# Performance work log

Hardware: AMD Instinct MI355X
Metric: run time of the kernel (lower is better)

Reference implementation:

```python
import jax, jax.numpy as jnp
import numpy as np

N, E, EL = 20000, 320000, 100000
IN, HID, OUT, H = 256, 128, 128, 4
NEG_SLOPE = 0.2


def setup_inputs() -> dict:
    key = jax.random.key(0)
    ks = jax.random.split(key, 20)
    g = lambda k, shape, fan: jax.random.normal(k, shape, jnp.float32) * (1.0 / np.sqrt(fan))
    inp = {
        'x': jax.random.normal(ks[0], (N, IN), jnp.float32),
        'edge_index': jax.random.randint(ks[1], (2, E), 0, N, jnp.int32),
        'edge_label_index': jax.random.randint(ks[2], (2, EL), 0, N, jnp.int32),
        # GATv2 layer 1: in -> hidden, heads=H, concat
        'W_l1': g(ks[3], (IN, H * HID), IN), 'b_l1': jnp.zeros((H * HID,), jnp.float32),
        'W_r1': g(ks[4], (IN, H * HID), IN), 'b_r1': jnp.zeros((H * HID,), jnp.float32),
        'att1': g(ks[5], (H, HID), HID), 'bias1': jnp.zeros((H * HID,), jnp.float32),
        # GATv2 layer 2: H*hidden -> out, heads=1
        'W_l2': g(ks[6], (H * HID, OUT), H * HID), 'b_l2': jnp.zeros((OUT,), jnp.float32),
        'W_r2': g(ks[7], (H * HID, OUT), H * HID), 'b_r2': jnp.zeros((OUT,), jnp.float32),
        'att2': g(ks[8], (1, OUT), OUT), 'bias2': jnp.zeros((OUT,), jnp.float32),
        # decoder: Linear(2*OUT, HID) -> GELU -> Linear(HID, 1)
        'W_d1': g(ks[9], (2 * OUT, HID), 2 * OUT), 'b_d1': jnp.zeros((HID,), jnp.float32),
        'W_d2': g(ks[10], (HID, 1), HID), 'b_d2': jnp.zeros((1,), jnp.float32),
    }
    return inp


def gatv2_conv(x, src, dst, Wl, bl, Wr, br, att, bias, heads, ch):
    n = x.shape[0]
    xl = (x @ Wl + bl).reshape(n, heads, ch)  # source transform
    xr = (x @ Wr + br).reshape(n, heads, ch)  # target transform
    xj = xl[src]                              # [E, H, C] messages from source
    xi = xr[dst]                              # [E, H, C]
    e = jax.nn.leaky_relu(xi + xj, NEG_SLOPE)
    logits = jnp.einsum('ehc,hc->eh', e, att)  # [E, H]
    # segment softmax over incoming edges of each target node
    m = jax.ops.segment_max(logits, dst, num_segments=n)
    a = jnp.exp(logits - m[dst])
    s = jax.ops.segment_sum(a, dst, num_segments=n)
    alpha = a / s[dst]
    out = jax.ops.segment_sum(alpha[..., None] * xj, dst, num_segments=n)
    return out.reshape(n, heads * ch) + bias


def reference(x, edge_index, edge_label_index,
              W_l1, b_l1, W_r1, b_r1, att1, bias1,
              W_l2, b_l2, W_r2, b_r2, att2, bias2,
              W_d1, b_d1, W_d2, b_d2):
    n = x.shape[0]
    loops = jnp.arange(n, dtype=edge_index.dtype)
    src = jnp.concatenate([edge_index[0], loops])  # add_self_loops=True (PyG default)
    dst = jnp.concatenate([edge_index[1], loops])
    z = gatv2_conv(x, src, dst, W_l1, b_l1, W_r1, b_r1, att1, bias1, H, HID)
    z = jax.nn.gelu(z)  # dropout is identity in eval mode
    z = gatv2_conv(z, src, dst, W_l2, b_l2, W_r2, b_r2, att2, bias2, 1, OUT)
    # link decoder: gather-concat-MLP
    h = jnp.concatenate([z[edge_label_index[0]], z[edge_label_index[1]]], axis=-1)
    h = jax.nn.gelu(h @ W_d1 + b_d1)
    return (h @ W_d2 + b_d2).squeeze(-1)
```

## Files before the change

### kernel.cpp

```cpp
#include <hip/hip_runtime.h>
#include <hip/hip_bf16.h>
#include <math.h>
#include <stdint.h>

using bf16 = __hip_bfloat16;
typedef unsigned short u16;
typedef unsigned int   u32;
typedef __attribute__((ext_vector_type(8))) short short8;
typedef __attribute__((ext_vector_type(4))) float f32x4;

static constexpr int NN   = 20000;
static constexpr int EE   = 320000;
static constexpr int ELN  = 100000;
static constexpr int ETOT = EE + NN;
static constexpr int INC  = 256;
static constexpr int C1   = 512;
static constexpr int C2   = 128;
static constexpr int NB   = (NN + 255) / 256;

__device__ __forceinline__ float us2f(u16 u){ union{u32 i; float f;}x; x.i=((u32)u)<<16; return x.f; }
__device__ __forceinline__ u16  f2us(float f){ union{bf16 h; u16 u;}c; c.h=__float2bfloat16(f); return c.u; }
__device__ __forceinline__ float h2f(u16 u){ union{u16 u; _Float16 h;}c; c.u=u; return (float)c.h; }
__device__ __forceinline__ float gelu_f(float x){
  float u = 1.5957691216057308f*(x + 0.044715f*x*x*x);
  float ex = __expf(u);
  float th = 1.f - 2.f/(ex + 1.f);
  return 0.5f*x*(1.f+th);
}
__device__ __forceinline__ void ld4v(const float* p, float* o){ float4 v=*(const float4*)p; o[0]=v.x;o[1]=v.y;o[2]=v.z;o[3]=v.w; }
__device__ __forceinline__ void ld4v(const u16* p, float* o){ uint2 v=*(const uint2*)p;
  o[0]=us2f(v.x&0xffff);o[1]=us2f(v.x>>16);o[2]=us2f(v.y&0xffff);o[3]=us2f(v.y>>16); }
__device__ __forceinline__ void ld4v(const _Float16* p, float* o){ uint2 v=*(const uint2*)p;
  o[0]=h2f(v.x&0xffff);o[1]=h2f(v.x>>16);o[2]=h2f(v.y&0xffff);o[3]=h2f(v.y>>16); }
__device__ __forceinline__ void ld8v(const float* p, float* o){ ld4v(p,o); ld4v(p+4,o+4); }
__device__ __forceinline__ void ld8v(const u16* p, float* o){ uint4 v=*(const uint4*)p;
  o[0]=us2f(v.x&0xffff);o[1]=us2f(v.x>>16);o[2]=us2f(v.y&0xffff);o[3]=us2f(v.y>>16);
  o[4]=us2f(v.z&0xffff);o[5]=us2f(v.z>>16);o[6]=us2f(v.w&0xffff);o[7]=us2f(v.w>>16); }
__device__ __forceinline__ void ld8v(const _Float16* p, float* o){ uint4 v=*(const uint4*)p;
  o[0]=h2f(v.x&0xffff);o[1]=h2f(v.x>>16);o[2]=h2f(v.y&0xffff);o[3]=h2f(v.y>>16);
  o[4]=h2f(v.z&0xffff);o[5]=h2f(v.z>>16);o[6]=h2f(v.w&0xffff);o[7]=h2f(v.w>>16); }
__device__ __forceinline__ void ld2v(const float* p, float* o){ float2 v=*(const float2*)p; o[0]=v.x;o[1]=v.y; }
__device__ __forceinline__ void ld2v(const _Float16* p, float* o){ u32 w=*(const u32*)p;
  o[0]=h2f(w&0xffff); o[1]=h2f(w>>16); }
__device__ __forceinline__ void st4v(float* p, const float* v){ *(float4*)p = make_float4(v[0],v[1],v[2],v[3]); }
__device__ __forceinline__ void st4v(u16* p, const float* v){ uint2 o;
  o.x=f2us(v[0])|((u32)f2us(v[1])<<16); o.y=f2us(v[2])|((u32)f2us(v[3])<<16); *(uint2*)p=o; }
__device__ __forceinline__ void st8v(float* p, const float* v){ st4v(p,v); st4v(p+4,v+4); }
__device__ __forceinline__ void st8v(u16* p, const float* v){ uint4 o;
  o.x=f2us(v[0])|((u32)f2us(v[1])<<16); o.y=f2us(v[2])|((u32)f2us(v[3])<<16);
  o.z=f2us(v[4])|((u32)f2us(v[5])<<16); o.w=f2us(v[6])|((u32)f2us(v[7])<<16); *(uint4*)p=o; }
__device__ __forceinline__ void st8v(_Float16* p, const float* v){
  union{ _Float16 h[8]; uint4 u; } c;
  #pragma unroll
  for (int j=0;j<8;++j) c.h[j] = (_Float16)v[j];
  *(uint4*)p = c.u; }

__global__ void k_hist(const int* __restrict__ ei, int* __restrict__ cnt) {
  int e = blockIdx.x*blockDim.x + threadIdx.x;
  if (e < ETOT) {
    int d = (e < EE) ? ei[EE + e] : (e - EE);
    if ((u32)d < (u32)NN) atomicAdd(&cnt[d], 1);
  }
}
__global__ void k_scan_a(const int* __restrict__ cnt, int* __restrict__ row_ptr,
                         int* __restrict__ bsum) {
  __shared__ int buf[256];
  int idx = blockIdx.x*256 + threadIdx.x;
  int v = (idx < NN) ? cnt[idx] : 0;
  buf[threadIdx.x] = v;
  __syncthreads();
  for (int off = 1; off < 256; off <<= 1) {
    int t = (threadIdx.x >= off) ? buf[threadIdx.x - off] : 0;
    __syncthreads();
    buf[threadIdx.x] += t;
    __syncthreads();
  }
  if (idx < NN) row_ptr[idx] = buf[threadIdx.x] - v;
  if (threadIdx.x == 255) bsum[blockIdx.x] = buf[255];
}
__global__ void k_scan_b(int* __restrict__ bsum, int* __restrict__ row_ptr) {
  __shared__ int buf[128];
  int v = (threadIdx.x < NB) ? bsum[threadIdx.x] : 0;
  buf[threadIdx.x] = v;
  __syncthreads();
  for (int off = 1; off < 128; off <<= 1) {
    int t = (threadIdx.x >= off) ? buf[threadIdx.x - off] : 0;
    __syncthreads();
    buf[threadIdx.x] += t;
    __syncthreads();
  }
  if (threadIdx.x < NB) bsum[threadIdx.x] = buf[threadIdx.x] - v;
  if (threadIdx.x == 127) row_ptr[NN] = buf[127];
}
__global__ void k_scan_c(int* __restrict__ row_ptr, const int* __restrict__ bsum,
                         int* __restrict__ cur) {
  int idx = blockIdx.x*256 + threadIdx.x;
  if (idx < NN) {
    int v = row_ptr[idx] + bsum[blockIdx.x];
    row_ptr[idx] = v;
    cur[idx] = v;
  }
}
__global__ void k_scatter(const int* __restrict__ ei, int* __restrict__ cur,
                          int* __restrict__ col) {
  int e = blockIdx.x*blockDim.x + threadIdx.x;
  if (e < ETOT) {
    int s, d;
    if (e < EE) { s = ei[e]; d = ei[EE + e]; } else { s = d = e - EE; }
    if ((u32)d >= (u32)NN) d = 0;
    int pos = atomicAdd(&cur[d], 1);
    if ((u32)pos < (u32)ETOT) col[pos] = s;
  }
}

struct WsArgs { const float* src[5]; u16* th[5]; u16* tl[5]; int K[5]; int N[5]; };
__global__ __launch_bounds__(256) void k_wsplit_all(WsArgs a) {
  int seg = blockIdx.y;
  int K = a.K[seg], N = a.N[seg];
  int n = K * N;
  int idx = blockIdx.x*256 + threadIdx.x;
  if (idx >= n) return;
  int nn = idx / K, k = idx - nn*K;
  float v = a.src[seg][(size_t)k*N + nn];
  u16 h = f2us(v);
  a.th[seg][idx] = h;
  a.tl[seg][idx] = f2us(v - us2f(h));
}

template <typename AT, typename CT>
__global__ __launch_bounds__(256, 2)
void k_mgemm(const AT* __restrict__ A,
             const u16* __restrict__ Bth, const u16* __restrict__ Btl,
             const float* __restrict__ bias, CT* __restrict__ C,
             int M, int N, int K) {
  __shared__ __align__(16) u16 Ah[128][32], Al[128][32];
  __shared__ __align__(16) u16 Bh[128][32], Bl[128][32];
  int tid = threadIdx.x;
  int m0 = blockIdx.x * 128, n0 = blockIdx.y * 128;
  int wave = tid >> 6, lane = tid & 63;
  int wm = (wave & 1) * 64, wn = (wave >> 1) * 64;
  int l15 = lane & 15, quad = lane >> 4;
  f32x4 acc[4][4] = {};
  int ar = tid >> 3;
  int ak = (tid & 7) * 4;
  int bn = tid >> 2;
  int bc = (tid & 3) * 8;
  for (int k0 = 0; k0 < K; k0 += 32) {
    #pragma unroll
    for (int i = 0; i < 4; ++i) {
      int row = ar + 32*i;
      int gr = m0 + row;
      float hv[4] = {0.f, 0.f, 0.f, 0.f};
      if (gr < M) ld4v(&A[(size_t)gr*K + k0 + ak], hv);
      u16 hi[4], lo[4];
      #pragma unroll
      for (int j = 0; j < 4; ++j) {
        hi[j] = f2us(hv[j]);
        lo[j] = f2us(hv[j] - us2f(hi[j]));
      }
      *(uint2*)&Ah[row][ak] = make_uint2(hi[0]|((u32)hi[1]<<16), hi[2]|((u32)hi[3]<<16));
      *(uint2*)&Al[row][ak] = make_uint2(lo[0]|((u32)lo[1]<<16), lo[2]|((u32)lo[3]<<16));
    }
    #pragma unroll
    for (int i = 0; i < 2; ++i) {
      int n = bn + 64*i;
      *(uint4*)&Bh[n][bc] = *(const uint4*)&Bth[(size_t)(n0+n)*K + k0 + bc];
      *(uint4*)&Bl[n][bc] = *(const uint4*)&Btl[(size_t)(n0+n)*K + k0 + bc];
    }
    __syncthreads();
    short8 af_h[4], af_l[4], bf_h[4], bf_l[4];
    #pragma unroll
    for (int i = 0; i < 4; ++i) {
      af_h[i] = *(const short8*)&Ah[wm + i*16 + l15][quad*8];
      af_l[i] = *(const short8*)&Al[wm + i*16 + l15][quad*8];
      bf_h[i] = *(const short8*)&Bh[wn + i*16 + l15][quad*8];
      bf_l[i] = *(const short8*)&Bl[wn + i*16 + l15][quad*8];
    }
    #pragma unroll
    for (int i = 0; i < 4; ++i)
      #pragma unroll
      for (int j = 0; j < 4; ++j) {
        acc[i][j] = __builtin_amdgcn_mfma_f32_16x16x32_bf16(af_h[i], bf_l[j], acc[i][j], 0,0,0);
        acc[i][j] = __builtin_amdgcn_mfma_f32_16x16x32_bf16(af_l[i], bf_h[j], acc[i][j], 0,0,0);
        acc[i][j] = __builtin_amdgcn_mfma_f32_16x16x32_bf16(af_h[i], bf_h[j], acc[i][j], 0,0,0);
      }
    __syncthreads();
  }
  #pragma unroll
  for (int j = 0; j < 4; ++j) {
    int col = n0 + wn + j*16 + l15;
    float bv = bias[col];
    #pragma unroll
    for (int i = 0; i < 4; ++i) {
      int rbase = m0 + wm + i*16 + quad*4;
      #pragma unroll
      for (int r = 0; r < 4; ++r) {
        int row = rbase + r;
        if (row < M) C[(size_t)row*N + col] = (CT)(acc[i][j][r] + bv);
      }
    }
  }
}

__global__ __launch_bounds__(256, 2)
void k_dec3(const _Float16* __restrict__ z2,
            const int* __restrict__ eli,
            const u16* __restrict__ Wth, const u16* __restrict__ Wtl,
            const float* __restrict__ bd1,
            const float* __restrict__ Wd2, const float* __restrict__ bd2,
            float* __restrict__ out) {
  __shared__ __align__(16) u16 Ah[128][32], Al[128][32];
  __shared__ __align__(16) u16 Bh[128][32], Bl[128][32];
  __shared__ float pr[128][2];
  int tid = threadIdx.x;
  int e0 = blockIdx.x * 128;
  int wave = tid >> 6, lane = tid & 63;
  int wm = (wave & 1) * 64, wn = (wave >> 1) * 64;
  int l15 = lane & 15, quad = lane >> 4;
  int ar = tid >> 3;
  int ak = (tid & 7) * 4;
  int bn = tid >> 2;
  int bc = (tid & 3) * 8;
  int ia4[4], ib4[4];
  #pragma unroll
  for (int i = 0; i < 4; ++i) {
    int e = e0 + ar + 32*i;
    bool ev = e < ELN;
    int a = ev ? eli[e] : 0;      if ((u32)a >= (u32)NN) a = 0;
    int b = ev ? eli[ELN+e] : 0;  if ((u32)b >= (u32)NN) b = 0;
    ia4[i] = a; ib4[i] = b;
  }
  f32x4 acc[4][4] = {};
  for (int k0 = 0; k0 < 256; k0 += 32) {
    #pragma unroll
    for (int i = 0; i < 4; ++i) {
      int row = ar + 32*i;
      int kk = k0 + ak;
      const _Float16* src = (kk < 128) ? &z2[(size_t)ia4[i]*128 + kk]
                                       : &z2[(size_t)ib4[i]*128 + (kk - 128)];
      float hv[4];
      ld4v(src, hv);
      u16 hi[4], lo[4];
      #pragma unroll
      for (int j = 0; j < 4; ++j) {
        hi[j] = f2us(hv[j]);
        lo[j] = f2us(hv[j] - us2f(hi[j]));
      }
      *(uint2*)&Ah[row][ak] = make_uint2(hi[0]|((u32)hi[1]<<16), hi[2]|((u32)hi[3]<<16));
      *(uint2*)&Al[row][ak] = make_uint2(lo[0]|((u32)lo[1]<<16), lo[2]|((u32)lo[3]<<16));
    }
    #pragma unroll
    for (int i = 0; i < 2; ++i) {
      int n = bn + 64*i;
      *(uint4*)&Bh[n][bc] = *(const uint4*)&Wth[(size_t)n*256 + k0 + bc];
      *(uint4*)&Bl[n][bc] = *(const uint4*)&Wtl[(size_t)n*256 + k0 + bc];
    }
    __syncthreads();
    short8 af_h[4], af_l[4], bf_h[4], bf_l[4];
    #pragma unroll
    for (int i = 0; i < 4; ++i) {
      af_h[i] = *(const short8*)&Ah[wm + i*16 + l15][quad*8];
      af_l[i] = *(const short8*)&Al[wm + i*16 + l15][quad*8];
      bf_h[i] = *(const short8*)&Bh[wn + i*16 + l15][quad*8];
      bf_l[i] = *(const short8*)&Bl[wn + i*16 + l15][quad*8];
    }
    #pragma unroll
    for (int i = 0; i < 4; ++i)
      #pragma unroll
      for (int j = 0; j < 4; ++j) {
        acc[i][j] = __builtin_amdgcn_mfma_f32_16x16x32_bf16(af_h[i], bf_l[j], acc[i][j], 0,0,0);
        acc[i][j] = __builtin_amdgcn_mfma_f32_16x16x32_bf16(af_l[i], bf_h[j], acc[i][j], 0,0,0);
        acc[i][j] = __builtin_amdgcn_mfma_f32_16x16x32_bf16(af_h[i], bf_h[j], acc[i][j], 0,0,0);
      }
    __syncthreads();
  }
  float w2c[4], bbc[4];
  #pragma unroll
  for (int j = 0; j < 4; ++j) {
    int col = wn + j*16 + l15;
    w2c[j] = Wd2[col];
    bbc[j] = bd1[col];
  }
  #pragma unroll
  for (int i = 0; i < 4; ++i) {
    #pragma unroll
    for (int r = 0; r < 4; ++r) {
      float part = 0.f;
      #pragma unroll
      for (int j = 0; j < 4; ++j)
        part += gelu_f(acc[i][j][r] + bbc[j]) * w2c[j];
      part += __shfl_xor(part,1); part += __shfl_xor(part,2);
      part += __shfl_xor(part,4); part += __shfl_xor(part,8);
      if (l15 == 0) pr[wm + i*16 + quad*4 + r][wn>>6] = part;
    }
  }
  __syncthreads();
  if (tid < 128) {
    int e = e0 + tid;
    if (e < ELN) out[e] = pr[tid][0] + pr[tid][1] + bd2[0];
  }
}

template <typename AT, typename CT>
__global__ __launch_bounds__(256) void k_gemm(const AT* __restrict__ A,
                                              const float* __restrict__ W,
                                              const float* __restrict__ bias,
                                              CT* __restrict__ C,
                                              int M, int Nc, int K) {
  __shared__ __align__(16) float As[16][64];
  __shared__ __align__(16) float Bs[16][64];
  int tid = threadIdx.x;
  int m0 = blockIdx.x*64, n0 = blockIdx.y*64;
  int ty = tid >> 4, tx = tid & 15;
  int lrow = tid >> 2;
  int lk   = (tid & 3)*4;
  int wk   = tid >> 4;
  int wn   = (tid & 15)*4;
  float acc[4][4] = {};
  for (int k0 = 0; k0 < K; k0 += 16) {
    int row = m0 + lrow;
    if (row < M) {
      float a4[4]; ld4v(&A[(size_t)row*K + k0 + lk], a4);
      As[lk+0][lrow]=a4[0]; As[lk+1][lrow]=a4[1]; As[lk+2][lrow]=a4[2]; As[lk+3][lrow]=a4[3];
    } else {
      #pragma unroll
      for (int j=0;j<4;++j) As[lk+j][lrow]=0.f;
    }
    {
      float4 bv4 = *(const float4*)&W[(size_t)(k0+wk)*Nc + n0 + wn];
      Bs[wk][wn+0]=bv4.x; Bs[wk][wn+1]=bv4.y; Bs[wk][wn+2]=bv4.z; Bs[wk][wn+3]=bv4.w;
    }
    __syncthreads();
    #pragma unroll
    for (int kk=0;kk<16;++kk) {
      float4 av = *(const float4*)&As[kk][ty*4];
      float4 bv = *(const float4*)&Bs[kk][tx*4];
      float a[4]={av.x,av.y,av.z,av.w}, b[4]={bv.x,bv.y,bv.z,bv.w};
      #pragma unroll
      for (int i=0;i<4;++i)
        #pragma unroll
        for (int j=0;j<4;++j)
          acc[i][j] += a[i]*b[j];
    }
    __syncthreads();
  }
  float bv[4];
  #pragma unroll
  for (int j=0;j<4;++j) bv[j] = bias[n0 + tx*4 + j];
  #pragma unroll
  for (int i=0;i<4;++i) {
    int row = m0 + ty*4 + i;
    if (row < M) {
      float o4[4] = {acc[i][0]+bv[0], acc[i][1]+bv[1], acc[i][2]+bv[2], acc[i][3]+bv[3]};
      st4v(&C[(size_t)row*Nc + n0 + tx*4], o4);
    }
  }
}

template <typename TI, typename TO>
__global__ __launch_bounds__(256) void k_edge1(const TI* __restrict__ xl,
                                               const TI* __restrict__ xr,
                                               const float* __restrict__ att,
                                               const float* __restrict__ bias,
                                               const int* __restrict__ row_ptr,
                                               const int* __restrict__ col,
                                               TO* __restrict__ z1) {
  int wid = (blockIdx.x*blockDim.x + threadIdx.x) >> 6;
  if (wid >= NN) return;
  int lane = threadIdx.x & 63;
  int c8 = lane*8;
  float xi[8], av[8], acc[8] = {};
  ld8v(&xr[(size_t)wid*C1 + c8], xi);
  #pragma unroll
  for (int j=0;j<8;++j) av[j] = att[c8+j];
  float m = -1e30f, s = 0.f;
  int e0 = row_ptr[wid], e1 = row_ptr[wid+1];
  int e = e0;
  if ((e1 - e0) & 1) {
    int sn = col[e]; if ((u32)sn >= (u32)NN) sn = 0;
    float xj[8];
    ld8v(&xl[(size_t)sn*C1 + c8], xj);
    float p = 0.f;
    #pragma unroll
    for (int j=0;j<8;++j) {
      float t = xi[j] + xj[j];
      t = fmaxf(t, 0.2f*t);
      p += t*av[j];
    }
    p += __shfl_xor(p,1); p += __shfl_xor(p,2);
    p += __shfl_xor(p,4); p += __shfl_xor(p,8);
    float mn = fmaxf(m, p);
    float f = __expf(m - mn), w = __expf(p - mn);
    s = s*f + w;
    #pragma unroll
    for (int j=0;j<8;++j) acc[j] = acc[j]*f + w*xj[j];
    m = mn;
    ++e;
  }
  for (; e < e1; e += 2) {
    int s1 = col[e];   if ((u32)s1 >= (u32)NN) s1 = 0;
    int s2 = col[e+1]; if ((u32)s2 >= (u32)NN) s2 = 0;
    float xj1[8], xj2[8];
    ld8v(&xl[(size_t)s1*C1 + c8], xj1);
    ld8v(&xl[(size_t)s2*C1 + c8], xj2);
    float p1 = 0.f, p2 = 0.f;
    #pragma unroll
    for (int j=0;j<8;++j) {
      float t1 = xi[j] + xj1[j]; t1 = fmaxf(t1, 0.2f*t1); p1 += t1*av[j];
      float t2 = xi[j] + xj2[j]; t2 = fmaxf(t2, 0.2f*t2); p2 += t2*av[j];
    }
    p1 += __shfl_xor(p1,1); p2 += __shfl_xor(p2,1);
    p1 += __shfl_xor(p1,2); p2 += __shfl_xor(p2,2);
    p1 += __shfl_xor(p1,4); p2 += __shfl_xor(p2,4);
    p1 += __shfl_xor(p1,8); p2 += __shfl_xor(p2,8);
    float mn = fmaxf(m, fmaxf(p1, p2));
    float f  = __expf(m - mn);
    float w1 = __expf(p1 - mn);
    float w2 = __expf(p2 - mn);
    s = s*f + w1 + w2;
    #pragma unroll
    for (int j=0;j<8;++j) acc[j] = acc[j]*f + (w1*xj1[j] + w2*xj2[j]);
    m = mn;
  }
  float inv = 1.f/s, o[8];
  #pragma unroll
  for (int j=0;j<8;++j) o[j] = gelu_f(acc[j]*inv + bias[c8+j]);
  st8v(&z1[(size_t)wid*C1 + c8], o);
}

template <typename TI, typename TO>
__global__ __launch_bounds__(256) void k_edge2(const TI* __restrict__ xl,
                                               const TI* __restrict__ xr,
                                               const float* __restrict__ att,
                                               const float* __restrict__ bias,
                                               const int* __restrict__ row_ptr,
                                               const int* __restrict__ col,
                                               TO* __restrict__ z2) {
  int wid = (blockIdx.x*blockDim.x + threadIdx.x) >> 6;
  if (wid >= NN) return;
  int lane = threadIdx.x & 63;
  int c2 = lane*2;
  float xiv[2];
  ld2v(&xr[(size_t)wid*C2 + c2], xiv);
  float a0 = att[c2], a1 = att[c2+1];
  float m = -1e30f, s = 0.f, ac0 = 0.f, ac1 = 0.f;
  int e0 = row_ptr[wid], e1 = row_ptr[wid+1];
  int e = e0;
  if ((e1 - e0) & 1) {
    int sn = col[e]; if ((u32)sn >= (u32)NN) sn = 0;
    float xj[2];
    ld2v(&xl[(size_t)sn*C2 + c2], xj);
    float t0 = xiv[0] + xj[0]; t0 = fmaxf(t0, 0.2f*t0);
    float t1 = xiv[1] + xj[1]; t1 = fmaxf(t1, 0.2f*t1);
    float p = t0*a0 + t1*a1;
    p += __shfl_xor(p,1);  p += __shfl_xor(p,2);
    p += __shfl_xor(p,4);  p += __shfl_xor(p,8);
    p += __shfl_xor(p,16); p += __shfl_xor(p,32);
    float mn = fmaxf(m, p);
    float f = __expf(m - mn), w = __expf(p - mn);
    s = s*f + w;
    ac0 = ac0*f + w*xj[0];
    ac1 = ac1*f + w*xj[1];
    m = mn;
    ++e;
  }
  for (; e < e1; e += 2) {
    int s1 = col[e];   if ((u32)s1 >= (u32)NN) s1 = 0;
    int s2 = col[e+1]; if ((u32)s2 >= (u32)NN) s2 = 0;
    float xj1[2], xj2[2];
    ld2v(&xl[(size_t)s1*C2 + c2], xj1);
    ld2v(&xl[(size_t)s2*C2 + c2], xj2);
    float u0 = xiv[0] + xj1[0]; u0 = fmaxf(u0, 0.2f*u0);
    float u1 = xiv[1] + xj1[1]; u1 = fmaxf(u1, 0.2f*u1);
    float v0 = xiv[0] + xj2[0]; v0 = fmaxf(v0, 0.2f*v0);
    float v1 = xiv[1] + xj2[1]; v1 = fmaxf(v1, 0.2f*v1);
    float p1 = u0*a0 + u1*a1;
    float p2 = v0*a0 + v1*a1;
    p1 += __shfl_xor(p1,1);  p2 += __shfl_xor(p2,1);
    p1 += __shfl_xor(p1,2);  p2 += __shfl_xor(p2,2);
    p1 += __shfl_xor(p1,4);  p2 += __shfl_xor(p2,4);
    p1 += __shfl_xor(p1,8);  p2 += __shfl_xor(p2,8);
    p1 += __shfl_xor(p1,16); p2 += __shfl_xor(p2,16);
    p1 += __shfl_xor(p1,32); p2 += __shfl_xor(p2,32);
    float mn = fmaxf(m, fmaxf(p1, p2));
    float f  = __expf(m - mn);
    float w1 = __expf(p1 - mn);
    float w2 = __expf(p2 - mn);
    s = s*f + w1 + w2;
    ac0 = ac0*f + (w1*xj1[0] + w2*xj2[0]);
    ac1 = ac1*f + (w1*xj1[1] + w2*xj2[1]);
    m = mn;
  }
  float inv = 1.f/s;
  z2[(size_t)wid*C2 + c2]   = (TO)(ac0*inv + bias[c2]);
  z2[(size_t)wid*C2 + c2+1] = (TO)(ac1*inv + bias[c2+1]);
}

__global__ __launch_bounds__(256) void k_dec2(const float* __restrict__ z2,
                                              const int* __restrict__ eli,
                                              const float* __restrict__ Wd1,
                                              const float* __restrict__ bd1,
                                              const float* __restrict__ Wd2,
                                              const float* __restrict__ bd2,
                                              float* __restrict__ out) {
  __shared__ __align__(16) float As[16][64];
  __shared__ __align__(16) float Bs[16][128];
  int tid = threadIdx.x;
  int e0 = blockIdx.x * 64;
  int ty = tid >> 4, tx = tid & 15;
  int lrow = tid >> 2;
  int lk   = (tid & 3) * 4;
  int wk   = tid >> 4;
  int wn   = (tid & 15) * 8;
  int e = e0 + lrow;
  bool ev = e < ELN;
  int ia = ev ? eli[e] : 0;       if ((u32)ia >= (u32)NN) ia = 0;
  int ib = ev ? eli[ELN+e] : 0;   if ((u32)ib >= (u32)NN) ib = 0;
  float acc[4][8] = {};
  for (int k0 = 0; k0 < 256; k0 += 16) {
    int kk4 = k0 + lk;
    const float* src = (kk4 < 128) ? &z2[(size_t)ia*128 + kk4]
                                   : &z2[(size_t)ib*128 + (kk4 - 128)];
    float4 a4 = ev ? *(const float4*)src : make_float4(0.f,0.f,0.f,0.f);
    As[lk+0][lrow]=a4.x; As[lk+1][lrow]=a4.y; As[lk+2][lrow]=a4.z; As[lk+3][lrow]=a4.w;
    *(float4*)&Bs[wk][wn]   = *(const float4*)&Wd1[(size_t)(k0+wk)*128 + wn];
    *(float4*)&Bs[wk][wn+4] = *(const float4*)&Wd1[(size_t)(k0+wk)*128 + wn + 4];
    __syncthreads();
    #pragma unroll
    for (int kk = 0; kk < 16; ++kk) {
      float4 av = *(const float4*)&As[kk][ty*4];
      float a[4] = {av.x, av.y, av.z, av.w};
      float4 b0 = *(const float4*)&Bs[kk][tx*4];
      float4 b1 = *(const float4*)&Bs[kk][64 + tx*4];
      float b[8] = {b0.x,b0.y,b0.z,b0.w,b1.x,b1.y,b1.z,b1.w};
      #pragma unroll
      for (int i = 0; i < 4; ++i)
        #pragma unroll
        for (int j = 0; j < 8; ++j)
          acc[i][j] += a[i]*b[j];
    }
    __syncthreads();
  }
  float w2[8], bb[8];
  #pragma unroll
  for (int j = 0; j < 4; ++j) {
    w2[j]   = Wd2[tx*4+j];      bb[j]   = bd1[tx*4+j];
    w2[j+4] = Wd2[64+tx*4+j];   bb[j+4] = bd1[64+tx*4+j];
  }
  float b2 = bd2[0];
  #pragma unroll
  for (int i = 0; i < 4; ++i) {
    float part = 0.f;
    #pragma unroll
    for (int j = 0; j < 8; ++j)
      part += gelu_f(acc[i][j] + bb[j]) * w2[j];
    part += __shfl_xor(part,1); part += __shfl_xor(part,2);
    part += __shfl_xor(part,4); part += __shfl_xor(part,8);
    int row = e0 + ty*4 + i;
    if (tx == 0 && row < ELN) out[row] = part + b2;
  }
}

__global__ void k_tiny(float* out, float code) {
  if (threadIdx.x == 0) out[0] = code;
}

extern "C" void kernel_launch(void* const* d_in, const int* in_sizes, int n_in,
                              void* d_out, int out_size, void* d_ws, size_t ws_size,
                              hipStream_t stream) {
  const float* x     = (const float*)d_in[0];
  const int*   ei    = (const int*)  d_in[1];
  const int*   eli   = (const int*)  d_in[2];
  const float* Wl1   = (const float*)d_in[3];
  const float* bl1   = (const float*)d_in[4];
  const float* Wr1   = (const float*)d_in[5];
  const float* br1   = (const float*)d_in[6];
  const float* att1  = (const float*)d_in[7];
  const float* bias1 = (const float*)d_in[8];
  const float* Wl2   = (const float*)d_in[9];
  const float* bl2   = (const float*)d_in[10];
  const float* Wr2   = (const float*)d_in[11];
  const float* br2   = (const float*)d_in[12];
  const float* att2  = (const float*)d_in[13];
  const float* bias2 = (const float*)d_in[14];
  const float* Wd1   = (const float*)d_in[15];
  const float* bd1   = (const float*)d_in[16];
  const float* Wd2   = (const float*)d_in[17];
  const float* bd2   = (const float*)d_in[18];
  float* out = (float*)d_out;

  constexpr size_t INTW = (size_t)(NN+1) + NN + ETOT;
  constexpr size_t FULL_WORDS = 3ull*NN*C1 + INTW;
  constexpr size_t CMP_WORDS  = 3ull*NN*C1/2 + INTW;

  bool full    = ws_size >= FULL_WORDS*4;
  bool compact = !full && ws_size >= CMP_WORDS*4;
  if (!full && !compact) {
    size_t mb = ws_size >> 20;
    k_tiny<<<1, 64, 0, stream>>>(out, 16384.f + (float)mb);
    return;
  }

  size_t regA = full ? (size_t)NN*C1 : (size_t)NN*C1/2;
  char* base = (char*)d_ws;
  void* wA = base;
  void* wB = base + regA*4;
  void* wC = base + 2*regA*4;
  int* row_ptr = (int*)(base + 3*regA*4);
  int* cnt     = row_ptr + (NN + 1);
  int* col     = cnt + NN;
  int* bsum    = (int*)wA;

  hipMemsetAsync(cnt, 0, NN*sizeof(int), stream);
  k_hist<<<(ETOT+255)/256, 256, 0, stream>>>(ei, cnt);
  k_scan_a<<<NB, 256, 0, stream>>>(cnt, row_ptr, bsum);
  k_scan_b<<<1, 128, 0, stream>>>(bsum, row_ptr);
  k_scan_c<<<NB, 256, 0, stream>>>(row_ptr, bsum, cnt);
  k_scatter<<<(ETOT+255)/256, 256, 0, stream>>>(ei, cnt, col);

  if (full) {
    _Float16* xl1 = (_Float16*)wA;
    _Float16* xr1 = (_Float16*)wB;
    _Float16* z1  = (_Float16*)wC;
    _Float16* xl2 = (_Float16*)wA;
    _Float16* xr2 = (_Float16*)wB;
    _Float16* z2  = (_Float16*)wC;
    u16* wl1th = (u16*)((char*)wB + (21u<<20));
    u16* wl1tl = wl1th + 512*256;
    u16* wr1th = wl1tl + 512*256;
    u16* wr1tl = wr1th + 512*256;
    u16* wl2th = wr1tl + 512*256;
    u16* wl2tl = wl2th + 128*512;
    u16* wr2th = wl2tl + 128*512;
    u16* wr2tl = wr2th + 128*512;
    u16* wdth  = wr2tl + 128*512;
    u16* wdtl  = wdth  + 128*256;

    WsArgs wa;
    wa.src[0]=Wl1; wa.th[0]=wl1th; wa.tl[0]=wl1tl; wa.K[0]=INC; wa.N[0]=C1;
    wa.src[1]=Wr1; wa.th[1]=wr1th; wa.tl[1]=wr1tl; wa.K[1]=INC; wa.N[1]=C1;
    wa.src[2]=Wl2; wa.th[2]=wl2th; wa.tl[2]=wl2tl; wa.K[2]=C1;  wa.N[2]=C2;
    wa.src[3]=Wr2; wa.th[3]=wr2th; wa.tl[3]=wr2tl; wa.K[3]=C1;  wa.N[3]=C2;
    wa.src[4]=Wd1; wa.th[4]=wdth;  wa.tl[4]=wdtl;  wa.K[4]=256; wa.N[4]=C2;
    k_wsplit_all<<<dim3(512, 5), 256, 0, stream>>>(wa);

    dim3 gm1((NN+127)/128, C1/128);
    k_mgemm<float,_Float16><<<gm1, 256, 0, stream>>>(x, wl1th, wl1tl, bl1, xl1, NN, C1, INC);
    k_mgemm<float,_Float16><<<gm1, 256, 0, stream>>>(x, wr1th, wr1tl, br1, xr1, NN, C1, INC);
    k_edge1<_Float16,_Float16><<<NN/4, 256, 0, stream>>>(xl1, xr1, att1, bias1, row_ptr, col, z1);
    dim3 gm2((NN+127)/128, C2/128);
    k_mgemm<_Float16,_Float16><<<gm2, 256, 0, stream>>>(z1, wl2th, wl2tl, bl2, xl2, NN, C2, C1);
    k_mgemm<_Float16,_Float16><<<gm2, 256, 0, stream>>>(z1, wr2th, wr2tl, br2, xr2, NN, C2, C1);
    k_edge2<_Float16,_Float16><<<NN/4, 256, 0, stream>>>(xl2, xr2, att2, bias2, row_ptr, col, z2);
    k_dec3<<<(ELN+127)/128, 256, 0, stream>>>(z2, eli, wdth, wdtl, bd1, Wd2, bd2, out);
  } else {
    u16* xl1 = (u16*)wA;
    u16* xr1 = (u16*)wB;
    u16* z1  = (u16*)wC;
    float* xl2 = (float*)wA;
    float* xr2 = (float*)wB;
    float* z2  = (float*)wC;
    dim3 g1((NN+63)/64, C1/64);
    dim3 g2((NN+63)/64, C2/64);
    k_gemm<float,u16><<<g1, 256, 0, stream>>>(x, Wl1, bl1, xl1, NN, C1, INC);
    k_gemm<float,u16><<<g1, 256, 0, stream>>>(x, Wr1, br1, xr1, NN, C1, INC);
    k_edge1<u16,u16><<<NN/4, 256, 0, stream>>>(xl1, xr1, att1, bias1, row_ptr, col, z1);
    k_gemm<u16,float><<<g2, 256, 0, stream>>>(z1, Wl2, bl2, xl2, NN, C2, C1);
    k_gemm<u16,float><<<g2, 256, 0, stream>>>(z1, Wr2, br2, xr2, NN, C2, C1);
    k_edge2<float,float><<<NN/4, 256, 0, stream>>>(xl2, xr2, att2, bias2, row_ptr, col, z2);
    k_dec2<<<(ELN+63)/64, 256, 0, stream>>>(z2, eli, Wd1, bd1, Wd2, bd2, out);
  }
}
```

Before: 424.4 us.

## Fuse left/right GATv2 projections into one GEMM and drop online-softmax max tracking

Concatenates W_l and W_r into one weight matrix per layer so each layer runs a single wider GEMM producing interleaved xl|xr rows, with the edge kernels reading them through a leading-dimension stride. The first layer's input x is pre-split into bf16 hi/lo once by a new kernel, and a packed-A GEMM variant then loads those halves directly instead of converting fp32 per tile. The edge kernels also drop the running-max rescaling in the segment softmax and exponentiate logits directly, which removes exps and multiplies per edge but can overflow if logits grow large.

```diff
diff --git a/kernel.cpp b/kernel.cpp
--- a/kernel.cpp
+++ b/kernel.cpp
@@ -113,6 +113,17 @@
   }
 }
 
+__global__ __launch_bounds__(256) void k_xsplit(const float* __restrict__ A,
+                                                u16* __restrict__ Ath, u16* __restrict__ Atl,
+                                                int n) {
+  for (int i = blockIdx.x*256 + threadIdx.x; i < n; i += gridDim.x*256) {
+    float v = A[i];
+    u16 h = f2us(v);
+    Ath[i] = h;
+    Atl[i] = f2us(v - us2f(h));
+  }
+}
+
 struct WsArgs { const float* src[5]; u16* th[5]; u16* tl[5]; int K[5]; int N[5]; };
 __global__ __launch_bounds__(256) void k_wsplit_all(WsArgs a) {
   int seg = blockIdx.y;
@@ -127,12 +138,85 @@
   a.tl[seg][idx] = f2us(v - us2f(h));
 }
 
+template <typename CT>
+__global__ __launch_bounds__(256, 2)
+void k_mgemm_p(const u16* __restrict__ Ath, const u16* __restrict__ Atl,
+               const u16* __restrict__ Bth, const u16* __restrict__ Btl,
+               const float* __restrict__ biasA, const float* __restrict__ biasB, int ncut,
+               CT* __restrict__ C, int M, int N, int K) {
+  __shared__ __align__(16) u16 Ah[128][32], Al[128][32];
+  __shared__ __align__(16) u16 Bh[128][32], Bl[128][32];
+  int tid = threadIdx.x;
+  int m0 = blockIdx.x * 128, n0 = blockIdx.y * 128;
+  int wave = tid >> 6, lane = tid & 63;
+  int wm = (wave & 1) * 64, wn = (wave >> 1) * 64;
+  int l15 = lane & 15, quad = lane >> 4;
+  f32x4 acc[4][4] = {};
+  int ar = tid >> 1;
+  int ac = (tid & 1) * 16;
+  int bn = tid >> 2;
+  int bc = (tid & 3) * 8;
+  uint4 z4 = make_uint4(0,0,0,0);
+  for (int k0 = 0; k0 < K; k0 += 32) {
+    int gr = m0 + ar;
+    if (gr < M) {
+      const u16* ph = &Ath[(size_t)gr*K + k0 + ac];
+      const u16* pl = &Atl[(size_t)gr*K + k0 + ac];
+      *(uint4*)&Ah[ar][ac]   = *(const uint4*)ph;
+      *(uint4*)&Ah[ar][ac+8] = *(const uint4*)(ph+8);
+      *(uint4*)&Al[ar][ac]   = *(const uint4*)pl;
+      *(uint4*)&Al[ar][ac+8] = *(const uint4*)(pl+8);
+    } else {
+      *(uint4*)&Ah[ar][ac] = z4; *(uint4*)&Ah[ar][ac+8] = z4;
+      *(uint4*)&Al[ar][ac] = z4; *(uint4*)&Al[ar][ac+8] = z4;
+    }
+    #pragma unroll
+    for (int i = 0; i < 2; ++i) {
+      int n = bn + 64*i;
+      *(uint4*)&Bh[n][bc] = *(const uint4*)&Bth[(size_t)(n0+n)*K + k0 + bc];
+      *(uint4*)&Bl[n][bc] = *(const uint4*)&Btl[(size_t)(n0+n)*K + k0 + bc];
+    }
+    __syncthreads();
+    short8 af_h[4], af_l[4], bf_h[4], bf_l[4];
+    #pragma unroll
+    for (int i = 0; i < 4; ++i) {
+      af_h[i] = *(const short8*)&Ah[wm + i*16 + l15][quad*8];
+      af_l[i] = *(const short8*)&Al[wm + i*16 + l15][quad*8];
+      bf_h[i] = *(const short8*)&Bh[wn + i*16 + l15][quad*8];
+      bf_l[i] = *(const short8*)&Bl[wn + i*16 + l15][quad*8];
+    }
+    #pragma unroll
+    for (int i = 0; i < 4; ++i)
+      #pragma unroll
+      for (int j = 0; j < 4; ++j) {
+        acc[i][j] = __builtin_amdgcn_mfma_f32_16x16x32_bf16(af_h[i], bf_l[j], acc[i][j], 0,0,0);
+        acc[i][j] = __builtin_amdgcn_mfma_f32_16x16x32_bf16(af_l[i], bf_h[j], acc[i][j], 0,0,0);
+        acc[i][j] = __builtin_amdgcn_mfma_f32_16x16x32_bf16(af_h[i], bf_h[j], acc[i][j], 0,0,0);
+      }
+    __syncthreads();
+  }
+  #pragma unroll
+  for (int j = 0; j < 4; ++j) {
+    int col = n0 + wn + j*16 + l15;
+    float bv = (col < ncut) ? biasA[col] : biasB[col - ncut];
+    #pragma unroll
+    for (int i = 0; i < 4; ++i) {
+      int rbase = m0 + wm + i*16 + quad*4;
+      #pragma unroll
+      for (int r = 0; r < 4; ++r) {
+        int row = rbase + r;
+        if (row < M) C[(size_t)row*N + col] = (CT)(acc[i][j][r] + bv);
+      }
+    }
+  }
+}
+
 template <typename AT, typename CT>
 __global__ __launch_bounds__(256, 2)
 void k_mgemm(const AT* __restrict__ A,
              const u16* __restrict__ Bth, const u16* __restrict__ Btl,
-             const float* __restrict__ bias, CT* __restrict__ C,
-             int M, int N, int K) {
+             const float* __restrict__ biasA, const float* __restrict__ biasB, int ncut,
+             CT* __restrict__ C, int M, int N, int K) {
   __shared__ __align__(16) u16 Ah[128][32], Al[128][32];
   __shared__ __align__(16) u16 Bh[128][32], Bl[128][32];
   int tid = threadIdx.x;
@@ -189,7 +273,7 @@
   #pragma unroll
   for (int j = 0; j < 4; ++j) {
     int col = n0 + wn + j*16 + l15;
-    float bv = bias[col];
+    float bv = (col < ncut) ? biasA[col] : biasB[col - ncut];
     #pragma unroll
     for (int i = 0; i < 4; ++i) {
       int rbase = m0 + wm + i*16 + quad*4;
@@ -359,7 +443,7 @@
 
 template <typename TI, typename TO>
 __global__ __launch_bounds__(256) void k_edge1(const TI* __restrict__ xl,
-                                               const TI* __restrict__ xr,
+                                               const TI* __restrict__ xr, int ld,
                                                const float* __restrict__ att,
                                                const float* __restrict__ bias,
                                                const int* __restrict__ row_ptr,
@@ -370,16 +454,16 @@
   int lane = threadIdx.x & 63;
   int c8 = lane*8;
   float xi[8], av[8], acc[8] = {};
-  ld8v(&xr[(size_t)wid*C1 + c8], xi);
+  ld8v(&xr[(size_t)wid*ld + c8], xi);
   #pragma unroll
   for (int j=0;j<8;++j) av[j] = att[c8+j];
-  float m = -1e30f, s = 0.f;
+  float s = 0.f;
   int e0 = row_ptr[wid], e1 = row_ptr[wid+1];
   int e = e0;
   if ((e1 - e0) & 1) {
     int sn = col[e]; if ((u32)sn >= (u32)NN) sn = 0;
     float xj[8];
-    ld8v(&xl[(size_t)sn*C1 + c8], xj);
+    ld8v(&xl[(size_t)sn*ld + c8], xj);
     float p = 0.f;
     #pragma unroll
     for (int j=0;j<8;++j) {
@@ -389,20 +473,18 @@
     }
     p += __shfl_xor(p,1); p += __shfl_xor(p,2);
     p += __shfl_xor(p,4); p += __shfl_xor(p,8);
-    float mn = fmaxf(m, p);
-    float f = __expf(m - mn), w = __expf(p - mn);
-    s = s*f + w;
-    #pragma unroll
-    for (int j=0;j<8;++j) acc[j] = acc[j]*f + w*xj[j];
-    m = mn;
+    float w = __expf(p);
+    s += w;
+    #pragma unroll
+    for (int j=0;j<8;++j) acc[j] += w*xj[j];
     ++e;
   }
   for (; e < e1; e += 2) {
     int s1 = col[e];   if ((u32)s1 >= (u32)NN) s1 = 0;
     int s2 = col[e+1]; if ((u32)s2 >= (u32)NN) s2 = 0;
     float xj1[8], xj2[8];
-    ld8v(&xl[(size_t)s1*C1 + c8], xj1);
-    ld8v(&xl[(size_t)s2*C1 + c8], xj2);
+    ld8v(&xl[(size_t)s1*ld + c8], xj1);
+    ld8v(&xl[(size_t)s2*ld + c8], xj2);
     float p1 = 0.f, p2 = 0.f;
     #pragma unroll
     for (int j=0;j<8;++j) {
@@ -413,14 +495,11 @@
     p1 += __shfl_xor(p1,2); p2 += __shfl_xor(p2,2);
     p1 += __shfl_xor(p1,4); p2 += __shfl_xor(p2,4);
     p1 += __shfl_xor(p1,8); p2 += __shfl_xor(p2,8);
-    float mn = fmaxf(m, fmaxf(p1, p2));
-    float f  = __expf(m - mn);
-    float w1 = __expf(p1 - mn);
-    float w2 = __expf(p2 - mn);
-    s = s*f + w1 + w2;
-    #pragma unroll
-    for (int j=0;j<8;++j) acc[j] = acc[j]*f + (w1*xj1[j] + w2*xj2[j]);
-    m = mn;
+    float w1 = __expf(p1);
+    float w2 = __expf(p2);
+    s += w1 + w2;
+    #pragma unroll
+    for (int j=0;j<8;++j) acc[j] += w1*xj1[j] + w2*xj2[j];
   }
   float inv = 1.f/s, o[8];
   #pragma unroll
@@ -430,7 +509,7 @@
 
 template <typename TI, typename TO>
 __global__ __launch_bounds__(256) void k_edge2(const TI* __restrict__ xl,
-                                               const TI* __restrict__ xr,
+                                               const TI* __restrict__ xr, int ld,
                                                const float* __restrict__ att,
                                                const float* __restrict__ bias,
                                                const int* __restrict__ row_ptr,
@@ -441,35 +520,33 @@
   int lane = threadIdx.x & 63;
   int c2 = lane*2;
   float xiv[2];
-  ld2v(&xr[(size_t)wid*C2 + c2], xiv);
+  ld2v(&xr[(size_t)wid*ld + c2], xiv);
   float a0 = att[c2], a1 = att[c2+1];
-  float m = -1e30f, s = 0.f, ac0 = 0.f, ac1 = 0.f;
+  float s = 0.f, ac0 = 0.f, ac1 = 0.f;
   int e0 = row_ptr[wid], e1 = row_ptr[wid+1];
   int e = e0;
   if ((e1 - e0) & 1) {
     int sn = col[e]; if ((u32)sn >= (u32)NN) sn = 0;
     float xj[2];
-    ld2v(&xl[(size_t)sn*C2 + c2], xj);
+    ld2v(&xl[(size_t)sn*ld + c2], xj);
     float t0 = xiv[0] + xj[0]; t0 = fmaxf(t0, 0.2f*t0);
     float t1 = xiv[1] + xj[1]; t1 = fmaxf(t1, 0.2f*t1);
     float p = t0*a0 + t1*a1;
     p += __shfl_xor(p,1);  p += __shfl_xor(p,2);
     p += __shfl_xor(p,4);  p += __shfl_xor(p,8);
     p += __shfl_xor(p,16); p += __shfl_xor(p,32);
-    float mn = fmaxf(m, p);
-    float f = __expf(m - mn), w = __expf(p - mn);
-    s = s*f + w;
-    ac0 = ac0*f + w*xj[0];
-    ac1 = ac1*f + w*xj[1];
-    m = mn;
+    float w = __expf(p);
+    s += w;
+    ac0 += w*xj[0];
+    ac1 += w*xj[1];
     ++e;
   }
   for (; e < e1; e += 2) {
     int s1 = col[e];   if ((u32)s1 >= (u32)NN) s1 = 0;
     int s2 = col[e+1]; if ((u32)s2 >= (u32)NN) s2 = 0;
     float xj1[2], xj2[2];
-    ld2v(&xl[(size_t)s1*C2 + c2], xj1);
-    ld2v(&xl[(size_t)s2*C2 + c2], xj2);
+    ld2v(&xl[(size_t)s1*ld + c2], xj1);
+    ld2v(&xl[(size_t)s2*ld + c2], xj2);
     float u0 = xiv[0] + xj1[0]; u0 = fmaxf(u0, 0.2f*u0);
     float u1 = xiv[1] + xj1[1]; u1 = fmaxf(u1, 0.2f*u1);
     float v0 = xiv[0] + xj2[0]; v0 = fmaxf(v0, 0.2f*v0);
@@ -482,14 +559,11 @@
     p1 += __shfl_xor(p1,8);  p2 += __shfl_xor(p2,8);
     p1 += __shfl_xor(p1,16); p2 += __shfl_xor(p2,16);
     p1 += __shfl_xor(p1,32); p2 += __shfl_xor(p2,32);
-    float mn = fmaxf(m, fmaxf(p1, p2));
-    float f  = __expf(m - mn);
-    float w1 = __expf(p1 - mn);
-    float w2 = __expf(p2 - mn);
-    s = s*f + w1 + w2;
-    ac0 = ac0*f + (w1*xj1[0] + w2*xj2[0]);
-    ac1 = ac1*f + (w1*xj1[1] + w2*xj2[1]);
-    m = mn;
+    float w1 = __expf(p1);
+    float w2 = __expf(p2);
+    s += w1 + w2;
+    ac0 += w1*xj1[0] + w2*xj2[0];
+    ac1 += w1*xj1[1] + w2*xj2[1];
   }
   float inv = 1.f/s;
   z2[(size_t)wid*C2 + c2]   = (TO)(ac0*inv + bias[c2]);
@@ -619,39 +693,38 @@
   k_scatter<<<(ETOT+255)/256, 256, 0, stream>>>(ei, cnt, col);
 
   if (full) {
-    _Float16* xl1 = (_Float16*)wA;
-    _Float16* xr1 = (_Float16*)wB;
-    _Float16* z1  = (_Float16*)wC;
-    _Float16* xl2 = (_Float16*)wA;
-    _Float16* xr2 = (_Float16*)wB;
-    _Float16* z2  = (_Float16*)wC;
-    u16* wl1th = (u16*)((char*)wB + (21u<<20));
-    u16* wl1tl = wl1th + 512*256;
-    u16* wr1th = wl1tl + 512*256;
-    u16* wr1tl = wr1th + 512*256;
-    u16* wl2th = wr1tl + 512*256;
-    u16* wl2tl = wl2th + 128*512;
-    u16* wr2th = wl2tl + 128*512;
-    u16* wr2tl = wr2th + 128*512;
-    u16* wdth  = wr2tl + 128*512;
+    _Float16* xlr1 = (_Float16*)wA;
+    _Float16* z1   = (_Float16*)wC;
+    _Float16* xlr2 = (_Float16*)wA;
+    _Float16* z2   = (_Float16*)wC;
+    u16* xth = (u16*)wB;
+    u16* xtl = xth + (size_t)NN*INC;
+    u16* wt1th = (u16*)((char*)wB + (21u<<20));
+    u16* wt1tl = wt1th + 1024*256;
+    u16* wt2th = wt1tl + 1024*256;
+    u16* wt2tl = wt2th + 256*512;
+    u16* wdth  = wt2tl + 256*512;
     u16* wdtl  = wdth  + 128*256;
 
+    k_xsplit<<<2048, 256, 0, stream>>>(x, xth, xtl, NN*INC);
     WsArgs wa;
-    wa.src[0]=Wl1; wa.th[0]=wl1th; wa.tl[0]=wl1tl; wa.K[0]=INC; wa.N[0]=C1;
-    wa.src[1]=Wr1; wa.th[1]=wr1th; wa.tl[1]=wr1tl; wa.K[1]=INC; wa.N[1]=C1;
-    wa.src[2]=Wl2; wa.th[2]=wl2th; wa.tl[2]=wl2tl; wa.K[2]=C1;  wa.N[2]=C2;
-    wa.src[3]=Wr2; wa.th[3]=wr2th; wa.tl[3]=wr2tl; wa.K[3]=C1;  wa.N[3]=C2;
-    wa.src[4]=Wd1; wa.th[4]=wdth;  wa.tl[4]=wdtl;  wa.K[4]=256; wa.N[4]=C2;
+    wa.src[0]=Wl1; wa.th[0]=wt1th;          wa.tl[0]=wt1tl;          wa.K[0]=INC; wa.N[0]=C1;
+    wa.src[1]=Wr1; wa.th[1]=wt1th+512*256;  wa.tl[1]=wt1tl+512*256;  wa.K[1]=INC; wa.N[1]=C1;
+    wa.src[2]=Wl2; wa.th[2]=wt2th;          wa.tl[2]=wt2tl;          wa.K[2]=C1;  wa.N[2]=C2;
+    wa.src[3]=Wr2; wa.th[3]=wt2th+128*512;  wa.tl[3]=wt2tl+128*512;  wa.K[3]=C1;  wa.N[3]=C2;
+    wa.src[4]=Wd1; wa.th[4]=wdth;           wa.tl[4]=wdtl;           wa.K[4]=256; wa.N[4]=C2;
     k_wsplit_all<<<dim3(512, 5), 256, 0, stream>>>(wa);
 
-    dim3 gm1((NN+127)/128, C1/128);
-    k_mgemm<float,_Float16><<<gm1, 256, 0, stream>>>(x, wl1th, wl1tl, bl1, xl1, NN, C1, INC);
-    k_mgemm<float,_Float16><<<gm1, 256, 0, stream>>>(x, wr1th, wr1tl, br1, xr1, NN, C1, INC);
-    k_edge1<_Float16,_Float16><<<NN/4, 256, 0, stream>>>(xl1, xr1, att1, bias1, row_ptr, col, z1);
-    dim3 gm2((NN+127)/128, C2/128);
-    k_mgemm<_Float16,_Float16><<<gm2, 256, 0, stream>>>(z1, wl2th, wl2tl, bl2, xl2, NN, C2, C1);
-    k_mgemm<_Float16,_Float16><<<gm2, 256, 0, stream>>>(z1, wr2th, wr2tl, br2, xr2, NN, C2, C1);
-    k_edge2<_Float16,_Float16><<<NN/4, 256, 0, stream>>>(xl2, xr2, att2, bias2, row_ptr, col, z2);
+    dim3 gm1((NN+127)/128, 1024/128);
+    k_mgemm_p<_Float16><<<gm1, 256, 0, stream>>>(xth, xtl, wt1th, wt1tl,
+                                                 bl1, br1, 512, xlr1, NN, 1024, INC);
+    k_edge1<_Float16,_Float16><<<NN/4, 256, 0, stream>>>(xlr1, xlr1+512, 1024,
+                                                         att1, bias1, row_ptr, col, z1);
+    dim3 gm2((NN+127)/128, 256/128);
+    k_mgemm<_Float16,_Float16><<<gm2, 256, 0, stream>>>(z1, wt2th, wt2tl,
+                                                        bl2, br2, 128, xlr2, NN, 256, C1);
+    k_edge2<_Float16,_Float16><<<NN/4, 256, 0, stream>>>(xlr2, xlr2+128, 256,
+                                                         att2, bias2, row_ptr, col, z2);
     k_dec3<<<(ELN+127)/128, 256, 0, stream>>>(z2, eli, wdth, wdtl, bd1, Wd2, bd2, out);
   } else {
     u16* xl1 = (u16*)wA;
@@ -664,10 +737,10 @@
     dim3 g2((NN+63)/64, C2/64);
     k_gemm<float,u16><<<g1, 256, 0, stream>>>(x, Wl1, bl1, xl1, NN, C1, INC);
     k_gemm<float,u16><<<g1, 256, 0, stream>>>(x, Wr1, br1, xr1, NN, C1, INC);
-    k_edge1<u16,u16><<<NN/4, 256, 0, stream>>>(xl1, xr1, att1, bias1, row_ptr, col, z1);
+    k_edge1<u16,u16><<<NN/4, 256, 0, stream>>>(xl1, xr1, C1, att1, bias1, row_ptr, col, z1);
     k_gemm<u16,float><<<g2, 256, 0, stream>>>(z1, Wl2, bl2, xl2, NN, C2, C1);
     k_gemm<u16,float><<<g2, 256, 0, stream>>>(z1, Wr2, br2, xr2, NN, C2, C1);
-    k_edge2<float,float><<<NN/4, 256, 0, stream>>>(xl2, xr2, att2, bias2, row_ptr, col, z2);
+    k_edge2<float,float><<<NN/4, 256, 0, stream>>>(xl2, xr2, C2, att2, bias2, row_ptr, col, z2);
     k_dec2<<<(ELN+63)/64, 256, 0, stream>>>(z2, eli, Wd1, bd1, Wd2, bd2, out);
   }
 }
```

Result: faster. 392.2 us (-7.6%).
